# Kernel tuning notes

Measured on AMD Instinct MI355X. Metric: run time of the kernel, lower is better.

Reference implementation:

```python
import jax, jax.numpy as jnp
import numpy as np

M_DIM, Z_DIM, C = 256, 128, 32
N, L = 512, 384


def setup_inputs() -> dict:
    key = jax.random.key(0)
    ks = jax.random.split(key, 9)
    s = 1.0 / np.sqrt(M_DIM)
    return {
        "m": jax.random.normal(ks[0], (N, L, M_DIM), dtype=jnp.float32),
        "ln_gamma": jnp.ones((M_DIM,), jnp.float32),
        "ln_beta": jnp.zeros((M_DIM,), jnp.float32),
        "w1": jax.random.normal(ks[1], (M_DIM, C), jnp.float32) * s,
        "b1": jnp.zeros((C,), jnp.float32),
        "w2": jax.random.normal(ks[2], (M_DIM, C), jnp.float32) * s,
        "b2": jnp.zeros((C,), jnp.float32),
        "w3": jax.random.normal(ks[3], (C * C, Z_DIM), jnp.float32) * (1.0 / np.sqrt(C * C)),
        "b3": jnp.zeros((Z_DIM,), jnp.float32),
    }


def _layernorm(x, gamma, beta, eps=1e-5):
    mu = jnp.mean(x, axis=-1, keepdims=True)
    var = jnp.mean(jnp.square(x - mu), axis=-1, keepdims=True)
    return (x - mu) * jax.lax.rsqrt(var + eps) * gamma + beta


def reference(m, ln_gamma, ln_beta, w1, b1, w2, b2, w3, b3):
    n = m.shape[0]
    o = _layernorm(m, ln_gamma, ln_beta)          # (N, L, D)
    a = o @ w2 + b2                                # (N, L, C)  linear2
    b = o @ w1 + b1                                # (N, L, C)  linear1
    # mean over N of outer products: reassociated as a single contraction over n
    op = jnp.einsum('nia,njb->ijab', a, b) / n     # (L, L, C, C)
    ll = op.shape[0]
    z = op.reshape(ll, ll, -1) @ w3 + b3           # (L, L, Z)
    return z
```

## Files before the change

### kernel.cpp

```cpp
#include <hip/hip_runtime.h>
#include <hip/hip_bf16.h>
#include <stdint.h>

#define L_DIM 384
#define MD    256
#define CC    32
#define ZD    128
#define NB    512
#define K2    1024
#define MROWS 12288

typedef __attribute__((ext_vector_type(4)))  float f32x4;
typedef __attribute__((ext_vector_type(8)))  short bf16x8;

#define PRIO1() __builtin_amdgcn_s_setprio(1)
#define PRIO0() __builtin_amdgcn_s_setprio(0)

__device__ __forceinline__ unsigned short f2bf(float x) {
    union { float f; unsigned u; } v; v.f = x;
    unsigned r = v.u + 0x7fffu + ((v.u >> 16) & 1u);
    return (unsigned short)(r >> 16);
}

__device__ __forceinline__ uint2 pack4(unsigned short a, unsigned short b,
                                       unsigned short c, unsigned short d) {
    uint2 r; r.x = (unsigned)a | ((unsigned)b << 16);
    r.y = (unsigned)c | ((unsigned)d << 16); return r;
}

__device__ __forceinline__ unsigned cvtpk(float lo, float hi) {
    unsigned r;
    asm("v_cvt_pk_bf16_f32 %0, %1, %2" : "=v"(r) : "v"(lo), "v"(hi));
    return r;
}

__global__ __launch_bounds__(256) void prep_kernel(
    const float* __restrict__ w1, const float* __restrict__ w2,
    const float* __restrict__ w3,
    unsigned short* __restrict__ w3frag, unsigned short* __restrict__ wfrag)
{
    int idx = blockIdx.x * 256 + threadIdx.x;
    if (idx < 131072) {
        int e = idx & 7, lane = (idx >> 3) & 63, zg = (idx >> 9) & 7, ks = idx >> 12;
        int k2p = ks * 32 + ((lane >> 4) << 3) + e;
        int wrow = (k2p & 31) * 32 + (k2p >> 5);
        int z  = zg * 16 + (lane & 15);
        w3frag[idx] = f2bf(w3[(size_t)wrow * ZD + z]);
    } else {
        int j = idx - 131072;
        int e = j & 7, lane = (j >> 3) & 63, nf = (j >> 9) & 3, ks = j >> 11;
        int c = nf * 16 + (lane & 15);
        int d = ks * 32 + ((lane >> 4) << 3) + e;
        float v = (c < CC) ? w2[d * CC + c] : w1[d * CC + (c - CC)];
        wfrag[j] = f2bf(v);
    }
}

__global__ __launch_bounds__(256, 4) void ln_proj_kernel(
    const float* __restrict__ mm, const float* __restrict__ gamma, const float* __restrict__ beta,
    const unsigned short* __restrict__ wfrag,
    const float* __restrict__ b1, const float* __restrict__ b2,
    unsigned short* __restrict__ At, unsigned short* __restrict__ Bt)
{
    __shared__ alignas(16) char o_b[32768];

    const int tid = threadIdx.x, wv = tid >> 6, lane = tid & 63;
    const int l0 = blockIdx.y * 2;
    const int n0 = blockIdx.x * 32;

    const int l_loc = wv >> 1;
    const int nbase = (wv & 1) << 4;
    const int l_g = l0 + l_loc;
    f32x4 g4 = *(const f32x4*)(gamma + lane * 4);
    f32x4 e4 = *(const f32x4*)(beta + lane * 4);

    #pragma unroll 4
    for (int r = 0; r < 16; ++r) {
        int row_loc = wv * 16 + r;
        int n_g = n0 + nbase + r;
        const float* src = mm + ((size_t)n_g * L_DIM + l_g) * MD + lane * 4;
        f32x4 x = *(const f32x4*)src;
        float s  = x[0] + x[1] + x[2] + x[3];
        float s2 = x[0]*x[0] + x[1]*x[1] + x[2]*x[2] + x[3]*x[3];
        #pragma unroll
        for (int off = 32; off > 0; off >>= 1) {
            s  += __shfl_xor(s,  off);
            s2 += __shfl_xor(s2, off);
        }
        float mu  = s * (1.0f / MD);
        float var = s2 * (1.0f / MD) - mu * mu;
        float rs  = rsqrtf(var + 1e-5f);
        unsigned short o0 = f2bf((x[0] - mu) * rs * g4[0] + e4[0]);
        unsigned short o1 = f2bf((x[1] - mu) * rs * g4[1] + e4[1]);
        unsigned short o2 = f2bf((x[2] - mu) * rs * g4[2] + e4[2]);
        unsigned short o3 = f2bf((x[3] - mu) * rs * g4[3] + e4[3]);
        *(uint2*)(o_b + row_loc * 512 + ((lane * 8) ^ ((row_loc & 7) << 4))) = pack4(o0, o1, o2, o3);
    }

    f32x4 acc[4] = {{0,0,0,0},{0,0,0,0},{0,0,0,0},{0,0,0,0}};
    const int lrow = lane & 15;
    const int kq16 = (lane >> 4) << 4;
    const int arow = wv * 16 + lrow;
    #pragma unroll
    for (int ks = 0; ks < 8; ++ks) {
        bf16x8 a = *(const bf16x8*)(o_b + arow * 512 + ((ks * 64 + kq16) ^ ((arow & 7) << 4)));
        #pragma unroll
        for (int nf = 0; nf < 4; ++nf) {
            bf16x8 b = *(const bf16x8*)(wfrag + (size_t)((ks * 4 + nf) * 64 + lane) * 8);
            acc[nf] = __builtin_amdgcn_mfma_f32_16x16x32_bf16(a, b, acc[nf], 0, 0, 0);
        }
    }

    const int rr0 = wv * 16 + ((lane >> 4) << 2);
    const int n_gw = n0 + (rr0 & 31);
    const int l_gw = l0 + (rr0 >> 5);
    #pragma unroll
    for (int nf = 0; nf < 4; ++nf) {
        int c = nf * 16 + lrow;
        float bias = (c < CC) ? b2[c] : b1[c - CC];
        uint2 pk = pack4(f2bf(acc[nf][0] + bias), f2bf(acc[nf][1] + bias),
                         f2bf(acc[nf][2] + bias), f2bf(acc[nf][3] + bias));
        int c31 = c & 31;
        int f = l_gw * 2 + (c31 >> 4);
        int lanep = (c31 & 15) + (((n_gw >> 3) & 3) << 4);
        size_t addr = ((size_t)(f * 16 + (n_gw >> 5)) * 64 + lanep) * 8 + (n_gw & 7);
        *(uint2*)(((c < CC) ? At : Bt) + addr) = pk;
    }
}

__global__ __launch_bounds__(512, 2) void opm_kernel(
    const unsigned short* __restrict__ Atf, const unsigned short* __restrict__ Btf,
    const unsigned short* __restrict__ w3frag, const float* __restrict__ b3,
    float* __restrict__ Z)
{
    __shared__ alignas(128) char smem[131072];

    const int tid = threadIdx.x, wv = tid >> 6, lane = tid & 63;

    const int lin = blockIdx.x;
    const int xcd = lin & 7, chunk = lin >> 3;
    const int i0 = (xcd * 6 + (chunk % 6)) * 256;
    const int j0 = (chunk / 6) * 256;

    const int lrow = lane & 15;
    const int wr = (wv >> 2) * 128, wc = (wv & 3) * 64;
    const int fa0 = __builtin_amdgcn_readfirstlane((i0 + wr) >> 4);
    const int fb0 = __builtin_amdgcn_readfirstlane((j0 + wc) >> 4);

    f32x4 acc[8][4] = {};
    bf16x8 av0[8], bv0[4], av1[8], bv1[4];

    auto loadSet = [&](bf16x8* av, bf16x8* bv, int s) {
        #pragma unroll
        for (int mf = 0; mf < 8; ++mf)
            av[mf] = *(const bf16x8*)(Atf + (size_t)((fa0 + mf) * 16 + s) * 512 + lane * 8);
        #pragma unroll
        for (int nf = 0; nf < 4; ++nf)
            bv[nf] = *(const bf16x8*)(Btf + (size_t)((fb0 + nf) * 16 + s) * 512 + lane * 8);
    };
    auto mmSet = [&](bf16x8* av, bf16x8* bv) {
        PRIO1();
        #pragma unroll
        for (int mf = 0; mf < 8; ++mf)
            #pragma unroll
            for (int nf = 0; nf < 4; ++nf)
                acc[mf][nf] = __builtin_amdgcn_mfma_f32_16x16x32_bf16(
                    av[mf], bv[nf], acc[mf][nf], 0, 0, 0);
        PRIO0();
    };

    loadSet(av0, bv0, 0);
    loadSet(av1, bv1, 1);

    #pragma unroll
    for (int s = 0; s < 16; ++s) {
        bf16x8* av = (s & 1) ? av1 : av0;
        bf16x8* bv = (s & 1) ? bv1 : bv0;
        mmSet(av, bv);
        if (s + 2 < 16) loadSet(av, bv, s + 2);
    }

    char* const opb = smem;
    const int lq = lane >> 4;
    const int zg = __builtin_amdgcn_readfirstlane(wv);
    const int zc = zg * 16 + lrow;

    auto ldW = [&](int ks) -> bf16x8 {
        return *(const bf16x8*)(w3frag + (size_t)((ks * 8 + zg) * 64 + lane) * 8);
    };
    auto ldP = [&](int rg, int ks) -> bf16x8 {
        int row = rg * 16 + lrow;
        int g = ks * 4 + lq;
        int b = g >> 2, jj = g & 3;
        int inner = (b * 64 + jj * 16) ^ (((b >> 1) & 7) << 4) ^ ((row & 7) << 4);
        return *(const bf16x8*)(opb + row * 2048 + inner);
    };

    bf16x8 wR0 = ldW(0), wR1 = ldW(1), wR2 = ldW(2), wR3 = ldW(3);

    const float scale = 1.0f / (float)NB;
    #pragma unroll
    for (int mf = 0; mf < 8; ++mf) {
        #pragma unroll
        for (int nf = 0; nf < 4; ++nf) {
            int col = wc + nf * 16 + lrow;
            int bcol = col & 31;
            int row = wr + mf * 16 + ((lane >> 4) << 2);
            int pl = ((row >> 5) << 3) | (col >> 5);
            int a0e = row & 31;
            int inner = (bcol * 64 + a0e * 2) ^ (((bcol >> 1) & 7) << 4) ^ ((pl & 7) << 4);
            uint2 pk;
            pk.x = cvtpk(acc[mf][nf][0] * scale, acc[mf][nf][1] * scale);
            pk.y = cvtpk(acc[mf][nf][2] * scale, acc[mf][nf][3] * scale);
            *(uint2*)(opb + pl * 2048 + inner) = pk;
        }
    }
    __syncthreads();

    f32x4 accP[4] = {};
    bf16x8 pA[4], pB[4];
    #pragma unroll
    for (int r = 0; r < 4; ++r) pA[r] = ldP(r, 0);
    #pragma unroll
    for (int r = 0; r < 4; ++r) pB[r] = ldP(r, 1);

    #pragma unroll
    for (int ks = 0; ks < 32; ++ks) {
        bf16x8 w = ((ks & 3) == 0) ? wR0 : ((ks & 3) == 1) ? wR1
                 : ((ks & 3) == 2) ? wR2 : wR3;
        bf16x8* pc = (ks & 1) ? pB : pA;
        PRIO1();
        accP[0] = __builtin_amdgcn_mfma_f32_16x16x32_bf16(pc[0], w, accP[0], 0, 0, 0);
        accP[1] = __builtin_amdgcn_mfma_f32_16x16x32_bf16(pc[1], w, accP[1], 0, 0, 0);
        accP[2] = __builtin_amdgcn_mfma_f32_16x16x32_bf16(pc[2], w, accP[2], 0, 0, 0);
        accP[3] = __builtin_amdgcn_mfma_f32_16x16x32_bf16(pc[3], w, accP[3], 0, 0, 0);
        PRIO0();
        if (ks + 4 < 32) {
            if ((ks & 3) == 0)      wR0 = ldW(ks + 4);
            else if ((ks & 3) == 1) wR1 = ldW(ks + 4);
            else if ((ks & 3) == 2) wR2 = ldW(ks + 4);
            else                    wR3 = ldW(ks + 4);
        }
        if (ks + 2 < 32) {
            #pragma unroll
            for (int r = 0; r < 4; ++r) pc[r] = ldP(r, ks + 2);
        }
    }

    const int pq = (lane >> 4) << 2;
    const float bias = b3[zc];
    #pragma unroll
    for (int pf = 0; pf < 4; ++pf) {
        #pragma unroll
        for (int rr = 0; rr < 4; ++rr) {
            int pl = pf * 16 + pq + rr;
            int ii = (i0 >> 5) + (pl >> 3);
            int jj = (j0 >> 5) + (pl & 7);
            Z[((size_t)ii * L_DIM + jj) * ZD + zc] = accP[pf][rr] + bias;
        }
    }
}

extern "C" void kernel_launch(void* const* d_in, const int* in_sizes, int n_in,
                              void* d_out, int out_size, void* d_ws, size_t ws_size,
                              hipStream_t stream)
{
    const float* mm    = (const float*)d_in[0];
    const float* gamma = (const float*)d_in[1];
    const float* beta  = (const float*)d_in[2];
    const float* w1    = (const float*)d_in[3];
    const float* b1    = (const float*)d_in[4];
    const float* w2    = (const float*)d_in[5];
    const float* b2    = (const float*)d_in[6];
    const float* w3    = (const float*)d_in[7];
    const float* b3    = (const float*)d_in[8];

    unsigned short* At     = (unsigned short*)d_ws;
    unsigned short* Bt     = At + (size_t)MROWS * NB;
    unsigned short* w3frag = Bt + (size_t)MROWS * NB;
    unsigned short* wfrag  = w3frag + 131072;

    prep_kernel<<<576, 256, 0, stream>>>(w1, w2, w3, w3frag, wfrag);
    ln_proj_kernel<<<dim3(16, 192), 256, 0, stream>>>(mm, gamma, beta, wfrag, b1, b2, At, Bt);
    opm_kernel<<<2304, 512, 0, stream>>>(At, Bt, w3frag, b3, (float*)d_out);
}
```

Before: 238.9 us.

## Switch outer-product GEMM to 32x32x16 MFMA with matching fragment layout

Replaces the 16x16x32 bf16 MFMA tiling of the outer-product accumulation with 32x32x16 MFMA instructions. The fragment layout written by the projection kernel is re-laid out (32-wide lanes, grouped by 16-row n chunks), and the LDS writeback of the accumulator is rewritten for the 32x32 output register mapping. The larger MFMA shape means fewer instructions and fewer operand loads per FLOP, at the cost of a different register layout and more complex epilogue indexing.

```diff
diff --git a/kernel.cpp b/kernel.cpp
--- a/kernel.cpp
+++ b/kernel.cpp
@@ -9,8 +9,10 @@
 #define NB    512
 #define K2    1024
 #define MROWS 12288
+#define NF32  384
 
 typedef __attribute__((ext_vector_type(4)))  float f32x4;
+typedef __attribute__((ext_vector_type(16))) float f32x16;
 typedef __attribute__((ext_vector_type(8)))  short bf16x8;
 
 #define PRIO1() __builtin_amdgcn_s_setprio(1)
@@ -121,9 +123,8 @@
         uint2 pk = pack4(f2bf(acc[nf][0] + bias), f2bf(acc[nf][1] + bias),
                          f2bf(acc[nf][2] + bias), f2bf(acc[nf][3] + bias));
         int c31 = c & 31;
-        int f = l_gw * 2 + (c31 >> 4);
-        int lanep = (c31 & 15) + (((n_gw >> 3) & 3) << 4);
-        size_t addr = ((size_t)(f * 16 + (n_gw >> 5)) * 64 + lanep) * 8 + (n_gw & 7);
+        int lanep = c31 + (((n_gw >> 3) & 1) << 5);
+        size_t addr = ((size_t)((n_gw >> 4) * NF32 + l_gw) * 64 + lanep) * 8 + (n_gw & 7);
         *(uint2*)(((c < CC) ? At : Bt) + addr) = pk;
     }
 }
@@ -144,28 +145,35 @@
 
     const int lrow = lane & 15;
     const int wr = (wv >> 2) * 128, wc = (wv & 3) * 64;
-    const int fa0 = __builtin_amdgcn_readfirstlane((i0 + wr) >> 4);
-    const int fb0 = __builtin_amdgcn_readfirstlane((j0 + wc) >> 4);
-
-    f32x4 acc[8][4] = {};
+    const int fa0 = __builtin_amdgcn_readfirstlane((i0 + wr) >> 5);
+    const int fb0 = __builtin_amdgcn_readfirstlane((j0 + wc) >> 5);
+
+    f32x16 acc[4][2] = {};
     bf16x8 av0[8], bv0[4], av1[8], bv1[4];
 
     auto loadSet = [&](bf16x8* av, bf16x8* bv, int s) {
         #pragma unroll
-        for (int mf = 0; mf < 8; ++mf)
-            av[mf] = *(const bf16x8*)(Atf + (size_t)((fa0 + mf) * 16 + s) * 512 + lane * 8);
-        #pragma unroll
-        for (int nf = 0; nf < 4; ++nf)
-            bv[nf] = *(const bf16x8*)(Btf + (size_t)((fb0 + nf) * 16 + s) * 512 + lane * 8);
+        for (int kk = 0; kk < 2; ++kk) {
+            #pragma unroll
+            for (int mf = 0; mf < 4; ++mf)
+                av[kk * 4 + mf] = *(const bf16x8*)(Atf +
+                    (size_t)((2 * s + kk) * NF32 + fa0 + mf) * 512 + lane * 8);
+            #pragma unroll
+            for (int nf = 0; nf < 2; ++nf)
+                bv[kk * 2 + nf] = *(const bf16x8*)(Btf +
+                    (size_t)((2 * s + kk) * NF32 + fb0 + nf) * 512 + lane * 8);
+        }
     };
     auto mmSet = [&](bf16x8* av, bf16x8* bv) {
         PRIO1();
         #pragma unroll
-        for (int mf = 0; mf < 8; ++mf)
-            #pragma unroll
-            for (int nf = 0; nf < 4; ++nf)
-                acc[mf][nf] = __builtin_amdgcn_mfma_f32_16x16x32_bf16(
-                    av[mf], bv[nf], acc[mf][nf], 0, 0, 0);
+        for (int kk = 0; kk < 2; ++kk)
+            #pragma unroll
+            for (int mf = 0; mf < 4; ++mf)
+                #pragma unroll
+                for (int nf = 0; nf < 2; ++nf)
+                    acc[mf][nf] = __builtin_amdgcn_mfma_f32_32x32x16_bf16(
+                        av[kk * 4 + mf], bv[kk * 2 + nf], acc[mf][nf], 0, 0, 0);
         PRIO0();
     };
 
@@ -199,20 +207,23 @@
     bf16x8 wR0 = ldW(0), wR1 = ldW(1), wR2 = ldW(2), wR3 = ldW(3);
 
     const float scale = 1.0f / (float)NB;
-    #pragma unroll
-    for (int mf = 0; mf < 8; ++mf) {
-        #pragma unroll
-        for (int nf = 0; nf < 4; ++nf) {
-            int col = wc + nf * 16 + lrow;
-            int bcol = col & 31;
-            int row = wr + mf * 16 + ((lane >> 4) << 2);
-            int pl = ((row >> 5) << 3) | (col >> 5);
-            int a0e = row & 31;
-            int inner = (bcol * 64 + a0e * 2) ^ (((bcol >> 1) & 7) << 4) ^ ((pl & 7) << 4);
-            uint2 pk;
-            pk.x = cvtpk(acc[mf][nf][0] * scale, acc[mf][nf][1] * scale);
-            pk.y = cvtpk(acc[mf][nf][2] * scale, acc[mf][nf][3] * scale);
-            *(uint2*)(opb + pl * 2048 + inner) = pk;
+    const int bcol = lane & 31;
+    const int hq4  = (lane >> 5) << 2;
+    #pragma unroll
+    for (int mf = 0; mf < 4; ++mf) {
+        #pragma unroll
+        for (int nf = 0; nf < 2; ++nf) {
+            int pl = (((wr >> 5) + mf) << 3) | ((wc >> 5) + nf);
+            int swp = (((bcol >> 1) & 7) << 4) ^ ((pl & 7) << 4);
+            #pragma unroll
+            for (int q = 0; q < 4; ++q) {
+                int a0e = q * 8 + hq4;
+                int inner = (bcol * 64 + a0e * 2) ^ swp;
+                uint2 pk;
+                pk.x = cvtpk(acc[mf][nf][4*q+0] * scale, acc[mf][nf][4*q+1] * scale);
+                pk.y = cvtpk(acc[mf][nf][4*q+2] * scale, acc[mf][nf][4*q+3] * scale);
+                *(uint2*)(opb + pl * 2048 + inner) = pk;
+            }
         }
     }
     __syncthreads();
```

Result: slower. 257.7 us (+7.9%).
